# Performance work log

Measured on AMD Instinct MI355X. Metric: run time of the kernel, lower is better.

Reference implementation:

```python
import jax, jax.numpy as jnp
import numpy as np

EMBED_DIM = 384
HEADS = 6
HEAD_DIM = EMBED_DIM // HEADS
WINDOW = 64
B, T, M = 256, 256, 128


def setup_inputs() -> dict:
    key = jax.random.key(0)
    ks = jax.random.split(key, 7)
    s = 0.02
    return {
        "x": jax.random.normal(ks[0], (B, T, EMBED_DIM), dtype=jnp.float32),
        "memory": jax.random.normal(ks[1], (M, EMBED_DIM), dtype=jnp.float32),
        "loss_mask": jnp.ones((B, T), dtype=jnp.float32),
        "qkv_w": jax.random.normal(ks[2], (3 * EMBED_DIM, EMBED_DIM), dtype=jnp.float32) * s,
        "qkv_b": jnp.zeros((3 * EMBED_DIM,), dtype=jnp.float32),
        "proj_w": jax.random.normal(ks[3], (EMBED_DIM, EMBED_DIM), dtype=jnp.float32) * s,
        "proj_b": jnp.zeros((EMBED_DIM,), dtype=jnp.float32),
        "gate": jnp.ones((EMBED_DIM,), dtype=jnp.float32),
    }


def reference(x, memory, loss_mask, qkv_w, qkv_b, proj_w, proj_b, gate):
    Bb, Tt, C = x.shape
    H, D, W = HEADS, HEAD_DIM, WINDOW
    Mm = memory.shape[0]
    T_total = Mm + Tt

    qkv = x @ qkv_w.T + qkv_b                     # [B, T, 3C]
    q, k, v = jnp.split(qkv, 3, axis=-1)
    mem = jnp.broadcast_to(memory[None], (Bb, Mm, C))
    k = jnp.concatenate([mem, k], axis=1)          # [B, M+T, C]
    v = jnp.concatenate([mem, v], axis=1)

    q = q.reshape(Bb, Tt, H, D)
    k = k.reshape(Bb, T_total, H, D)
    v = v.reshape(Bb, T_total, H, D)

    att = jnp.einsum('bthd,bshd->bhts', q, k) * (1.0 / np.sqrt(D))  # [B,H,T,M+T]

    # memory prefix columns are fully attended; self-block is causal AND local-window
    i = jnp.arange(Tt)[:, None]
    j = jnp.arange(Tt)[None, :]
    self_mask = (j <= i) & (jnp.abs(i - j) <= W)   # [T, T]
    full_mask = jnp.concatenate(
        [jnp.ones((Tt, Mm), dtype=bool), self_mask], axis=1)  # [T, M+T]
    att = jnp.where(full_mask[None, None], att, -jnp.inf)
    att = jax.nn.softmax(att, axis=-1)

    out = jnp.einsum('bhts,bshd->bthd', att, v).reshape(Bb, Tt, C)
    out = (out * gate) @ proj_w.T + proj_b
    out = out * loss_mask[..., None]
    return out
```

## Files before the change

kernel.cpp:

```cpp
#include <hip/hip_runtime.h>
#include <hip/hip_bf16.h>

#define Bb 256
#define Tt 256
#define Cc 384
#define Hh 6
#define Dd 64
#define Ww 64
#define Mm 128

typedef short short8 __attribute__((ext_vector_type(8)));
typedef float floatx4 __attribute__((ext_vector_type(4)));

static __device__ __forceinline__ unsigned short f2bf(float f) {
  union { __hip_bfloat16 h; unsigned short u; } cvt;
  cvt.h = __float2bfloat16(f);
  return cvt.u;
}

static __device__ __forceinline__ void gl2lds16(const unsigned short* g, unsigned short* l) {
  __builtin_amdgcn_global_load_lds(
      (const __attribute__((address_space(1))) unsigned int*)(const void*)g,
      (__attribute__((address_space(3))) unsigned int*)(void*)l,
      16, 0, 0);
}


__global__ __launch_bounds__(256) void cvt_x(const float4* __restrict__ x,
                                             ushort4* __restrict__ xb) {
  size_t i = (size_t)blockIdx.x * 256 + threadIdx.x;
  float4 v = x[i];
  ushort4 o;
  o.x = f2bf(v.x); o.y = f2bf(v.y); o.z = f2bf(v.z); o.w = f2bf(v.w);
  xb[i] = o;
}

__global__ __launch_bounds__(256) void cvt_misc(const float* __restrict__ qkv_w,
                                                const float* __restrict__ proj_w,
                                                const float* __restrict__ mem,
                                                unsigned short* __restrict__ wb,
                                                unsigned short* __restrict__ pwb,
                                                unsigned short* __restrict__ memk,
                                                unsigned short* __restrict__ memvt) {
  int i = blockIdx.x * 256 + threadIdx.x;
  wb[i] = f2bf(qkv_w[i]);
  if (i < 147456) pwb[i] = f2bf(proj_w[i]);
  if (i < 49152) {
    int m = i / Cc, c = i % Cc, h = c >> 6, d = c & 63;
    unsigned short bv = f2bf(mem[i]);
    memk[(h * Mm + m) * Dd + d] = bv;
    memvt[(h * Dd + d) * Mm + m] = bv;
  }
}


__global__ __launch_bounds__(256) void gemm_qkv(const unsigned short* __restrict__ xb,
                                                const unsigned short* __restrict__ wb,
                                                const float* __restrict__ qkv_b,
                                                unsigned short* __restrict__ q,
                                                unsigned short* __restrict__ k,
                                                unsigned short* __restrict__ vt)
{
  int tid = threadIdx.x;
  int w = tid >> 6, lane = tid & 63, quad = lane >> 4, l16 = lane & 15;
  int rowbase = blockIdx.y * 128;
  int colbase = blockIdx.x * 128;
  int rowofs = (w >> 1) * 64, colofs = (w & 1) * 64;

  __shared__ __align__(16) unsigned short Alds[128 * 32];
  __shared__ __align__(16) unsigned short Blds[128 * 32];

  int srow = lane >> 2;
  int skc = (lane & 3) * 8;

  floatx4 acc[4][4] = {};
  for (int ks = 0; ks < 12; ++ks) {
    int kk = ks * 32;
#pragma unroll
    for (int c = w; c < 8; c += 4) {
      gl2lds16(xb + (size_t)(rowbase + c * 16 + srow) * 384 + kk + skc,
               &Alds[c * 512 + lane * 8]);
      gl2lds16(wb + (size_t)(colbase + c * 16 + srow) * 384 + kk + skc,
               &Blds[c * 512 + lane * 8]);
    }
    __syncthreads();

    short8 a[4], b[4];
#pragma unroll
    for (int rt = 0; rt < 4; ++rt)
      a[rt] = *reinterpret_cast<const short8*>(&Alds[(rowofs + rt * 16 + l16) * 32 + quad * 8]);
#pragma unroll
    for (int nt = 0; nt < 4; ++nt)
      b[nt] = *reinterpret_cast<const short8*>(&Blds[(colofs + nt * 16 + l16) * 32 + quad * 8]);
#pragma unroll
    for (int rt = 0; rt < 4; ++rt)
#pragma unroll
      for (int nt = 0; nt < 4; ++nt)
        acc[rt][nt] = __builtin_amdgcn_mfma_f32_16x16x32_bf16(a[rt], b[nt], acc[rt][nt], 0, 0, 0);
    __syncthreads();
  }

#pragma unroll
  for (int nt = 0; nt < 4; ++nt) {
    int col = colbase + colofs + nt * 16 + l16;
    int which = col >= 768 ? 2 : (col >= 384 ? 1 : 0);
    int cc = col - which * 384;
    int h = cc >> 6, d = cc & 63;
    float bias = qkv_b[col];
#pragma unroll
    for (int rt = 0; rt < 4; ++rt) {
#pragma unroll
      for (int r = 0; r < 4; ++r) {
        int row = rowbase + rowofs + rt * 16 + quad * 4 + r;
        int bidx = row >> 8, t = row & 255;
        float val = acc[rt][nt][r] + bias;
        size_t bh = (size_t)bidx * Hh + h;
        if (which == 0) {
          q[(bh * Tt + t) * Dd + d] = f2bf(val * 0.125f);
        } else if (which == 1) {
          k[(bh * Tt + t) * Dd + d] = f2bf(val);
        } else {
          vt[(bh * Dd + d) * Tt + t] = f2bf(val);
        }
      }
    }
  }
}

#define PSTRIDE 264

__global__ __launch_bounds__(256, 2) void attn(const unsigned short* __restrict__ q,
                                               const unsigned short* __restrict__ k,
                                               const unsigned short* __restrict__ vt,
                                               const unsigned short* __restrict__ memk,
                                               const unsigned short* __restrict__ memvt,
                                               const float* __restrict__ gate,
                                               unsigned short* __restrict__ aout)
{
  int tq = blockIdx.x, h = blockIdx.y, b = blockIdx.z;
  int t0 = tq * 64;
  int tid = threadIdx.x, w = tid >> 6, lane = tid & 63, quad = lane >> 4, l16 = lane & 15;

  size_t bh = (size_t)b * Hh + h;
  const unsigned short* qp = q + (bh * Tt + t0 + w * 16) * Dd;
  const unsigned short* kp = k + bh * Tt * Dd;
  const unsigned short* vp = vt + bh * Dd * Tt;
  const unsigned short* mkp = memk + (size_t)h * Mm * Dd;
  const unsigned short* mvp = memvt + (size_t)h * Dd * Mm;

  __shared__ __align__(16) unsigned short lds[33280];
  unsigned short* Kmem = lds;
  unsigned short* Kwin = lds + 8192;
  unsigned short* Pb   = lds;
  unsigned short* Vmem = lds + 16896;
  unsigned short* Vwin = lds + 25088;
  unsigned short* pw = Pb + w * 16 * PSTRIDE;

  short8 qa[2];
#pragma unroll
  for (int ks = 0; ks < 2; ++ks)
    qa[ks] = *reinterpret_cast<const short8*>(qp + l16 * Dd + ks * 32 + quad * 8);

#pragma unroll
  for (int i = 0; i < 4; ++i) {
    int G = (i * 4 + w) * 64;
    int g = G + lane;
    int r = g >> 3, cs = g & 7;
    int c = cs ^ (r & 7);
    gl2lds16(mkp + r * 64 + c * 8, Kmem + G * 8 + lane * 8);
  }
#pragma unroll
  for (int i = 0; i < 4; ++i) {
    int G = (i * 4 + w) * 64;
    int g = G + lane;
    int r = g >> 3, cs = g & 7;
    int c = cs ^ (r & 7);
    int j = t0 - 64 + r;
    if (j < 0) j = 0;
    gl2lds16(kp + (size_t)j * 64 + c * 8, Kwin + G * 8 + lane * 8);
  }
#pragma unroll
  for (int i = 0; i < 4; ++i) {
    int G = (i * 4 + w) * 64;
    int g = G + lane;
    int d = g >> 4, cs = g & 15;
    int c = (cs & 8) | ((cs & 7) ^ (d & 7));
    gl2lds16(mvp + d * Mm + c * 8, Vmem + G * 8 + lane * 8);
  }
#pragma unroll
  for (int i = 0; i < 4; ++i) {
    int G = (i * 4 + w) * 64;
    int g = G + lane;
    int d = g >> 4, cs = g & 15;
    int c = (cs & 8) | ((cs & 7) ^ (d & 7));
    int j0 = t0 - 64 + c * 8;
    if (j0 < 0) j0 = 0;
    gl2lds16(vp + (size_t)d * Tt + j0, Vwin + G * 8 + lane * 8);
  }
  __syncthreads();

  floatx4 s[16] = {};

#pragma unroll
  for (int ct = 0; ct < 8; ++ct)
#pragma unroll
    for (int ks = 0; ks < 2; ++ks) {
      int slot = (ks * 4 + quad) ^ (l16 & 7);
      short8 bf = *reinterpret_cast<const short8*>(Kmem + (ct * 16 + l16) * 64 + slot * 8);
      s[ct] = __builtin_amdgcn_mfma_f32_16x16x32_bf16(qa[ks], bf, s[ct], 0, 0, 0);
    }
#pragma unroll
  for (int ct = 0; ct < 8; ++ct) {
    if (ct >= w && ct <= w + 4) {
#pragma unroll
      for (int ks = 0; ks < 2; ++ks) {
        int slot = (ks * 4 + quad) ^ (l16 & 7);
        short8 bf = *reinterpret_cast<const short8*>(Kwin + (ct * 16 + l16) * 64 + slot * 8);
        s[8 + ct] = __builtin_amdgcn_mfma_f32_16x16x32_bf16(qa[ks], bf, s[8 + ct], 0, 0, 0);
      }
    }
  }
  __syncthreads();

#pragma unroll
  for (int ct = 8; ct < 16; ++ct) {
    int j = t0 - 64 + (ct - 8) * 16 + l16;
#pragma unroll
    for (int r = 0; r < 4; ++r) {
      int i = t0 + w * 16 + quad * 4 + r;
      bool valid = (j >= 0) && (j <= i) && (i - j <= 64);
      if (!valid) s[ct][r] = -1e30f;
    }
  }

  float rm[4], rs[4], inv[4];
#pragma unroll
  for (int r = 0; r < 4; ++r) {
    float m = -1e30f;
#pragma unroll
    for (int ct = 0; ct < 16; ++ct) m = fmaxf(m, s[ct][r]);
    rm[r] = m;
  }
#pragma unroll
  for (int off = 1; off < 16; off <<= 1)
#pragma unroll
    for (int r = 0; r < 4; ++r) rm[r] = fmaxf(rm[r], __shfl_xor(rm[r], off, 64));
#pragma unroll
  for (int r = 0; r < 4; ++r) {
    float sum = 0.f;
#pragma unroll
    for (int ct = 0; ct < 16; ++ct) {
      float p = __expf(s[ct][r] - rm[r]);
      s[ct][r] = p;
      sum += p;
    }
    rs[r] = sum;
  }
#pragma unroll
  for (int off = 1; off < 16; off <<= 1)
#pragma unroll
    for (int r = 0; r < 4; ++r) rs[r] += __shfl_xor(rs[r], off, 64);
#pragma unroll
  for (int r = 0; r < 4; ++r) inv[r] = 1.0f / rs[r];

#pragma unroll
  for (int ct = 0; ct < 16; ++ct)
#pragma unroll
    for (int r = 0; r < 4; ++r)
      pw[(quad * 4 + r) * PSTRIDE + ct * 16 + l16] = f2bf(s[ct][r]);

  floatx4 o[4] = {};
#pragma unroll
  for (int ks = 0; ks < 4; ++ks) {
    short8 pa = *reinterpret_cast<const short8*>(pw + l16 * PSTRIDE + ks * 32 + quad * 8);
#pragma unroll
    for (int dt = 0; dt < 4; ++dt) {
      int c0 = ks * 4 + quad;
      int slot = (c0 & 8) | ((c0 & 7) ^ (l16 & 7));
      short8 vb = *reinterpret_cast<const short8*>(Vmem + (dt * 16 + l16) * 128 + slot * 8);
      o[dt] = __builtin_amdgcn_mfma_f32_16x16x32_bf16(pa, vb, o[dt], 0, 0, 0);
    }
  }
#pragma unroll
  for (int ks = 0; ks < 4; ++ks) {
    if (ks >= (w >> 1) && ks <= 2 + (w >> 1)) {
      short8 pa = *reinterpret_cast<const short8*>(pw + l16 * PSTRIDE + (4 + ks) * 32 + quad * 8);
#pragma unroll
      for (int dt = 0; dt < 4; ++dt) {
        int c0 = ks * 4 + quad;
        int slot = (c0 & 8) | ((c0 & 7) ^ (l16 & 7));
        short8 vb = *reinterpret_cast<const short8*>(Vwin + (dt * 16 + l16) * 128 + slot * 8);
        o[dt] = __builtin_amdgcn_mfma_f32_16x16x32_bf16(pa, vb, o[dt], 0, 0, 0);
      }
    }
  }

#pragma unroll
  for (int dt = 0; dt < 4; ++dt) {
    int c = h * 64 + dt * 16 + l16;
    float g = gate[c];
#pragma unroll
    for (int r = 0; r < 4; ++r) {
      int t = t0 + w * 16 + quad * 4 + r;
      float val = o[dt][r] * inv[r] * g;
      aout[((size_t)b * Tt + t) * Cc + c] = f2bf(val);
    }
  }
}


__global__ __launch_bounds__(256) void gemm_proj(const unsigned short* __restrict__ ab,
                                                 const unsigned short* __restrict__ pwb,
                                                 const float* __restrict__ proj_b,
                                                 const float* __restrict__ loss_mask,
                                                 float* __restrict__ out)
{
  int tid = threadIdx.x;
  int w = tid >> 6, lane = tid & 63, quad = lane >> 4, l16 = lane & 15;
  int rowbase = blockIdx.y * 128;
  int colbase = blockIdx.x * 128;
  int rowofs = (w >> 1) * 64, colofs = (w & 1) * 64;

  __shared__ __align__(16) unsigned short Alds[128 * 32];
  __shared__ __align__(16) unsigned short Blds[128 * 32];

  int srow = lane >> 2;
  int skc = (lane & 3) * 8;

  floatx4 acc[4][4] = {};
  for (int ks = 0; ks < 12; ++ks) {
    int kk = ks * 32;
#pragma unroll
    for (int c = w; c < 8; c += 4) {
      gl2lds16(ab + (size_t)(rowbase + c * 16 + srow) * 384 + kk + skc,
               &Alds[c * 512 + lane * 8]);
      gl2lds16(pwb + (size_t)(colbase + c * 16 + srow) * 384 + kk + skc,
               &Blds[c * 512 + lane * 8]);
    }
    __syncthreads();

    short8 a[4], b[4];
#pragma unroll
    for (int rt = 0; rt < 4; ++rt)
      a[rt] = *reinterpret_cast<const short8*>(&Alds[(rowofs + rt * 16 + l16) * 32 + quad * 8]);
#pragma unroll
    for (int nt = 0; nt < 4; ++nt)
      b[nt] = *reinterpret_cast<const short8*>(&Blds[(colofs + nt * 16 + l16) * 32 + quad * 8]);
#pragma unroll
    for (int rt = 0; rt < 4; ++rt)
#pragma unroll
      for (int nt = 0; nt < 4; ++nt)
        acc[rt][nt] = __builtin_amdgcn_mfma_f32_16x16x32_bf16(a[rt], b[nt], acc[rt][nt], 0, 0, 0);
    __syncthreads();
  }

#pragma unroll
  for (int nt = 0; nt < 4; ++nt) {
    int col = colbase + colofs + nt * 16 + l16;
    float bias = proj_b[col];
#pragma unroll
    for (int rt = 0; rt < 4; ++rt) {
#pragma unroll
      for (int r = 0; r < 4; ++r) {
        int row = rowbase + rowofs + rt * 16 + quad * 4 + r;
        float val = (acc[rt][nt][r] + bias) * loss_mask[row];
        out[(size_t)row * 384 + col] = val;
      }
    }
  }
}


extern "C" void kernel_launch(void* const* d_in, const int* in_sizes, int n_in,
                              void* d_out, int out_size, void* d_ws, size_t ws_size,
                              hipStream_t stream) {
  const float* x = (const float*)d_in[0];
  const float* memory = (const float*)d_in[1];
  const float* loss_mask = (const float*)d_in[2];
  const float* qkv_w = (const float*)d_in[3];
  const float* qkv_b = (const float*)d_in[4];
  const float* proj_w = (const float*)d_in[5];
  const float* proj_b = (const float*)d_in[6];
  const float* gate = (const float*)d_in[7];
  float* out = (float*)d_out;

  char* ws = (char*)d_ws;
  unsigned short* xb    = (unsigned short*)(ws + 0);
  unsigned short* qb    = (unsigned short*)(ws + 50331648);
  unsigned short* kb    = (unsigned short*)(ws + 100663296);
  unsigned short* vtb   = (unsigned short*)(ws + 150994944);
  unsigned short* wb    = (unsigned short*)(ws + 201326592);
  unsigned short* pwb   = (unsigned short*)(ws + 202211328);
  unsigned short* memk  = (unsigned short*)(ws + 202506240);
  unsigned short* memvt = (unsigned short*)(ws + 202604544);
  unsigned short* aout  = xb;

  cvt_x<<<dim3(24576), dim3(256), 0, stream>>>((const float4*)x, (ushort4*)xb);
  cvt_misc<<<dim3(1728), dim3(256), 0, stream>>>(qkv_w, proj_w, memory, wb, pwb, memk, memvt);
  gemm_qkv<<<dim3(9, 512), dim3(256), 0, stream>>>(xb, wb, qkv_b, qb, kb, vtb);
  attn<<<dim3(4, 6, 256), dim3(256), 0, stream>>>(qb, kb, vtb, memk, memvt, gate, aout);
  gemm_proj<<<dim3(3, 512), dim3(256), 0, stream>>>(aout, pwb, proj_b, loss_mask, out);
}
```

Before: 468.6 us.

## Double-buffer LDS tiles and remap block IDs in QKV and projection GEMMs

Both GEMM kernels now keep two LDS buffers, so the global-to-LDS load for the next K slice is issued while MFMAs run on the current one. This halves the barriers per K step and hides load latency behind compute. Block indices are also permuted with an XCD-style round-robin remap (orig&7) so blocks that are consecutive in logical order land on the same die and can share L2. LDS use per block doubles, which may reduce occupancy.

Result: faster. 436.7 us (-6.8%).

```diff
diff --git a/kernel.cpp b/kernel.cpp
--- a/kernel.cpp
+++ b/kernel.cpp
@@ -63,40 +63,60 @@
 {
   int tid = threadIdx.x;
   int w = tid >> 6, lane = tid & 63, quad = lane >> 4, l16 = lane & 15;
-  int rowbase = blockIdx.y * 128;
-  int colbase = blockIdx.x * 128;
+
+  int orig = blockIdx.y * 9 + blockIdx.x;
+  int newid = (orig & 7) * 576 + (orig >> 3);
+  int bx = newid % 9, by = newid / 9;
+
+  int rowbase = by * 128;
+  int colbase = bx * 128;
   int rowofs = (w >> 1) * 64, colofs = (w & 1) * 64;
 
-  __shared__ __align__(16) unsigned short Alds[128 * 32];
-  __shared__ __align__(16) unsigned short Blds[128 * 32];
+  __shared__ __align__(16) unsigned short Alds[2][128 * 32];
+  __shared__ __align__(16) unsigned short Blds[2][128 * 32];
 
   int srow = lane >> 2;
   int skc = (lane & 3) * 8;
 
+#define STAGE_QKV(buf, ks_) do {                                                  \
+    int kk = (ks_) * 32;                                                          \
+    _Pragma("unroll")                                                             \
+    for (int c = w; c < 8; c += 4) {                                              \
+      gl2lds16(xb + (size_t)(rowbase + c * 16 + srow) * 384 + kk + skc,           \
+               &Alds[buf][c * 512 + lane * 8]);                                   \
+      gl2lds16(wb + (size_t)(colbase + c * 16 + srow) * 384 + kk + skc,           \
+               &Blds[buf][c * 512 + lane * 8]);                                   \
+    }                                                                             \
+  } while (0)
+
+#define COMPUTE_QKV(buf) do {                                                     \
+    short8 a[4], b[4];                                                            \
+    _Pragma("unroll")                                                             \
+    for (int rt = 0; rt < 4; ++rt)                                                \
+      a[rt] = *reinterpret_cast<const short8*>(                                   \
+          &Alds[buf][(rowofs + rt * 16 + l16) * 32 + quad * 8]);                  \
+    _Pragma("unroll")                                                             \
+    for (int nt = 0; nt < 4; ++nt)                                                \
+      b[nt] = *reinterpret_cast<const short8*>(                                   \
+          &Blds[buf][(colofs + nt * 16 + l16) * 32 + quad * 8]);                  \
+    _Pragma("unroll")                                                             \
+    for (int rt = 0; rt < 4; ++rt)                                                \
+      _Pragma("unroll")                                                           \
+      for (int nt = 0; nt < 4; ++nt)                                              \
+        acc[rt][nt] = __builtin_amdgcn_mfma_f32_16x16x32_bf16(a[rt], b[nt],       \
+                                                              acc[rt][nt], 0, 0, 0); \
+  } while (0)
+
   floatx4 acc[4][4] = {};
-  for (int ks = 0; ks < 12; ++ks) {
-    int kk = ks * 32;
-#pragma unroll
-    for (int c = w; c < 8; c += 4) {
-      gl2lds16(xb + (size_t)(rowbase + c * 16 + srow) * 384 + kk + skc,
-               &Alds[c * 512 + lane * 8]);
-      gl2lds16(wb + (size_t)(colbase + c * 16 + srow) * 384 + kk + skc,
-               &Blds[c * 512 + lane * 8]);
-    }
+  STAGE_QKV(0, 0);
+  __syncthreads();
+#pragma unroll
+  for (int ks = 0; ks < 12; ks += 2) {
+    STAGE_QKV(1, ks + 1);
+    COMPUTE_QKV(0);
     __syncthreads();
-
-    short8 a[4], b[4];
-#pragma unroll
-    for (int rt = 0; rt < 4; ++rt)
-      a[rt] = *reinterpret_cast<const short8*>(&Alds[(rowofs + rt * 16 + l16) * 32 + quad * 8]);
-#pragma unroll
-    for (int nt = 0; nt < 4; ++nt)
-      b[nt] = *reinterpret_cast<const short8*>(&Blds[(colofs + nt * 16 + l16) * 32 + quad * 8]);
-#pragma unroll
-    for (int rt = 0; rt < 4; ++rt)
-#pragma unroll
-      for (int nt = 0; nt < 4; ++nt)
-        acc[rt][nt] = __builtin_amdgcn_mfma_f32_16x16x32_bf16(a[rt], b[nt], acc[rt][nt], 0, 0, 0);
+    if (ks + 2 < 12) STAGE_QKV(0, ks + 2);
+    COMPUTE_QKV(1);
     __syncthreads();
   }
 
@@ -125,6 +145,8 @@
       }
     }
   }
+#undef STAGE_QKV
+#undef COMPUTE_QKV
 }
 
 #define PSTRIDE 264
@@ -317,40 +339,60 @@
 {
   int tid = threadIdx.x;
   int w = tid >> 6, lane = tid & 63, quad = lane >> 4, l16 = lane & 15;
-  int rowbase = blockIdx.y * 128;
-  int colbase = blockIdx.x * 128;
+
+  int orig = blockIdx.y * 3 + blockIdx.x;
+  int newid = (orig & 7) * 192 + (orig >> 3);
+  int bx = newid % 3, by = newid / 3;
+
+  int rowbase = by * 128;
+  int colbase = bx * 128;
   int rowofs = (w >> 1) * 64, colofs = (w & 1) * 64;
 
-  __shared__ __align__(16) unsigned short Alds[128 * 32];
-  __shared__ __align__(16) unsigned short Blds[128 * 32];
+  __shared__ __align__(16) unsigned short Alds[2][128 * 32];
+  __shared__ __align__(16) unsigned short Blds[2][128 * 32];
 
   int srow = lane >> 2;
   int skc = (lane & 3) * 8;
 
+#define STAGE_PROJ(buf, ks_) do {                                                 \
+    int kk = (ks_) * 32;                                                          \
+    _Pragma("unroll")                                                             \
+    for (int c = w; c < 8; c += 4) {                                              \
+      gl2lds16(ab + (size_t)(rowbase + c * 16 + srow) * 384 + kk + skc,           \
+               &Alds[buf][c * 512 + lane * 8]);                                   \
+      gl2lds16(pwb + (size_t)(colbase + c * 16 + srow) * 384 + kk + skc,          \
+               &Blds[buf][c * 512 + lane * 8]);                                   \
+    }                                                                             \
+  } while (0)
+
+#define COMPUTE_PROJ(buf) do {                                                    \
+    short8 a[4], b[4];                                                            \
+    _Pragma("unroll")                                                             \
+    for (int rt = 0; rt < 4; ++rt)                                                \
+      a[rt] = *reinterpret_cast<const short8*>(                                   \
+          &Alds[buf][(rowofs + rt * 16 + l16) * 32 + quad * 8]);                  \
+    _Pragma("unroll")                                                             \
+    for (int nt = 0; nt < 4; ++nt)                                                \
+      b[nt] = *reinterpret_cast<const short8*>(                                   \
+          &Blds[buf][(colofs + nt * 16 + l16) * 32 + quad * 8]);                  \
+    _Pragma("unroll")                                                             \
+    for (int rt = 0; rt < 4; ++rt)                                                \
+      _Pragma("unroll")                                                           \
+      for (int nt = 0; nt < 4; ++nt)                                              \
+        acc[rt][nt] = __builtin_amdgcn_mfma_f32_16x16x32_bf16(a[rt], b[nt],       \
+                                                              acc[rt][nt], 0, 0, 0); \
+  } while (0)
+
   floatx4 acc[4][4] = {};
-  for (int ks = 0; ks < 12; ++ks) {
-    int kk = ks * 32;
-#pragma unroll
-    for (int c = w; c < 8; c += 4) {
-      gl2lds16(ab + (size_t)(rowbase + c * 16 + srow) * 384 + kk + skc,
-               &Alds[c * 512 + lane * 8]);
-      gl2lds16(pwb + (size_t)(colbase + c * 16 + srow) * 384 + kk + skc,
-               &Blds[c * 512 + lane * 8]);
-    }
+  STAGE_PROJ(0, 0);
+  __syncthreads();
+#pragma unroll
+  for (int ks = 0; ks < 12; ks += 2) {
+    STAGE_PROJ(1, ks + 1);
+    COMPUTE_PROJ(0);
     __syncthreads();
-
-    short8 a[4], b[4];
-#pragma unroll
-    for (int rt = 0; rt < 4; ++rt)
-      a[rt] = *reinterpret_cast<const short8*>(&Alds[(rowofs + rt * 16 + l16) * 32 + quad * 8]);
-#pragma unroll
-    for (int nt = 0; nt < 4; ++nt)
-      b[nt] = *reinterpret_cast<const short8*>(&Blds[(colofs + nt * 16 + l16) * 32 + quad * 8]);
-#pragma unroll
-    for (int rt = 0; rt < 4; ++rt)
-#pragma unroll
-      for (int nt = 0; nt < 4; ++nt)
-        acc[rt][nt] = __builtin_amdgcn_mfma_f32_16x16x32_bf16(a[rt], b[nt], acc[rt][nt], 0, 0, 0);
+    if (ks + 2 < 12) STAGE_PROJ(0, ks + 2);
+    COMPUTE_PROJ(1);
     __syncthreads();
   }
 
@@ -368,6 +410,8 @@
       }
     }
   }
+#undef STAGE_PROJ
+#undef COMPUTE_PROJ
 }
 
 
```

## Restructure QKV and proj GEMMs with resident full-K weight tile and swizzled LDS

Applied to the files above, without the earlier changes.

Both GEMMs now load the whole 128-column by full-K weight tile into LDS once per block and stream 64-row activation tiles. The next A tile is prefetched while the epilogue stores run. LDS uses an XOR swizzle to avoid bank conflicts, blocks grow to 512 threads with setprio around the MFMA loops, and block IDs are remapped for XCD-aware scheduling. This cuts per-k-step barriers and repeated weight loads, at the cost of about 144KB of LDS per block, which limits occupancy to one block per CU.

Measured after the change: 446.3 us. -4.8%, faster.

```diff
diff --git a/kernel.cpp b/kernel.cpp
--- a/kernel.cpp
+++ b/kernel.cpp
@@ -24,6 +24,9 @@
       (__attribute__((address_space(3))) unsigned int*)(void*)l,
       16, 0, 0);
 }
+
+#define VW(N) asm volatile("s_waitcnt vmcnt(" #N ")" ::: "memory")
+#define BAR() __builtin_amdgcn_s_barrier()
 
 
 __global__ __launch_bounds__(256) void cvt_x(const float4* __restrict__ x,
@@ -54,7 +57,7 @@
 }
 
 
-__global__ __launch_bounds__(256) void gemm_qkv(const unsigned short* __restrict__ xb,
+__global__ __launch_bounds__(512) void gemm_qkv(const unsigned short* __restrict__ xb,
                                                 const unsigned short* __restrict__ wb,
                                                 const float* __restrict__ qkv_b,
                                                 unsigned short* __restrict__ q,
@@ -63,67 +66,98 @@
 {
   int tid = threadIdx.x;
   int w = tid >> 6, lane = tid & 63, quad = lane >> 4, l16 = lane & 15;
-  int rowbase = blockIdx.y * 128;
-  int colbase = blockIdx.x * 128;
-  int rowofs = (w >> 1) * 64, colofs = (w & 1) * 64;
-
-  __shared__ __align__(16) unsigned short Alds[128 * 32];
-  __shared__ __align__(16) unsigned short Blds[128 * 32];
-
-  int srow = lane >> 2;
-  int skc = (lane & 3) * 8;
-
-  floatx4 acc[4][4] = {};
-  for (int ks = 0; ks < 12; ++ks) {
-    int kk = ks * 32;
-#pragma unroll
-    for (int c = w; c < 8; c += 4) {
-      gl2lds16(xb + (size_t)(rowbase + c * 16 + srow) * 384 + kk + skc,
-               &Alds[c * 512 + lane * 8]);
-      gl2lds16(wb + (size_t)(colbase + c * 16 + srow) * 384 + kk + skc,
-               &Blds[c * 512 + lane * 8]);
-    }
-    __syncthreads();
-
-    short8 a[4], b[4];
-#pragma unroll
-    for (int rt = 0; rt < 4; ++rt)
-      a[rt] = *reinterpret_cast<const short8*>(&Alds[(rowofs + rt * 16 + l16) * 32 + quad * 8]);
-#pragma unroll
-    for (int nt = 0; nt < 4; ++nt)
-      b[nt] = *reinterpret_cast<const short8*>(&Blds[(colofs + nt * 16 + l16) * 32 + quad * 8]);
-#pragma unroll
-    for (int rt = 0; rt < 4; ++rt)
-#pragma unroll
-      for (int nt = 0; nt < 4; ++nt)
-        acc[rt][nt] = __builtin_amdgcn_mfma_f32_16x16x32_bf16(a[rt], b[nt], acc[rt][nt], 0, 0, 0);
-    __syncthreads();
-  }
-
-#pragma unroll
-  for (int nt = 0; nt < 4; ++nt) {
-    int col = colbase + colofs + nt * 16 + l16;
-    int which = col >= 768 ? 2 : (col >= 384 ? 1 : 0);
-    int cc = col - which * 384;
-    int h = cc >> 6, d = cc & 63;
-    float bias = qkv_b[col];
-#pragma unroll
-    for (int rt = 0; rt < 4; ++rt) {
-#pragma unroll
-      for (int r = 0; r < 4; ++r) {
-        int row = rowbase + rowofs + rt * 16 + quad * 4 + r;
-        int bidx = row >> 8, t = row & 255;
-        float val = acc[rt][nt][r] + bias;
-        size_t bh = (size_t)bidx * Hh + h;
-        if (which == 0) {
-          q[(bh * Tt + t) * Dd + d] = f2bf(val * 0.125f);
-        } else if (which == 1) {
-          k[(bh * Tt + t) * Dd + d] = f2bf(val);
-        } else {
-          vt[(bh * Dd + d) * Tt + t] = f2bf(val);
+
+  int id = blockIdx.y * 9 + blockIdx.x;
+  int orig = (id & 7) * 288 + (id >> 3);
+  int bx = orig % 9, by = orig / 9;
+  int colbase = bx * 128;
+  int rowbase0 = by * 256;
+  int rowofs = (w >> 2) * 32, colofs = (w & 3) * 32;
+
+  __shared__ __align__(16) unsigned short Bl[49152];
+  __shared__ __align__(16) unsigned short Al[24576];
+
+#pragma unroll
+  for (int i = 0; i < 12; ++i) {
+    int G = i * 512 + tid;
+    int kg = G >> 10, g = G & 1023;
+    int col = g >> 3, cs = g & 7, c = cs ^ (col & 7);
+    gl2lds16(wb + (size_t)(colbase + col) * 384 + kg * 64 + c * 8, Bl + G * 8);
+  }
+#pragma unroll
+  for (int i = 0; i < 6; ++i) {
+    int G = i * 512 + tid;
+    int kg = G >> 9, g = G & 511;
+    int r = g >> 3, cs = g & 7, c = cs ^ (r & 7);
+    gl2lds16(xb + (size_t)(rowbase0 + r) * 384 + kg * 64 + c * 8, Al + G * 8);
+  }
+  VW(0); BAR();
+
+#pragma unroll
+  for (int t = 0; t < 4; ++t) {
+    floatx4 acc[2][2] = {};
+    __builtin_amdgcn_s_setprio(1);
+#pragma unroll
+    for (int kg = 0; kg < 6; ++kg) {
+#pragma unroll
+      for (int ks = 0; ks < 2; ++ks) {
+        int slot = ((ks * 4 + quad) ^ (l16 & 7)) * 8;
+        short8 a[2], b[2];
+#pragma unroll
+        for (int rt = 0; rt < 2; ++rt)
+          a[rt] = *reinterpret_cast<const short8*>(
+              &Al[kg * 4096 + (rowofs + rt * 16 + l16) * 64 + slot]);
+#pragma unroll
+        for (int nt = 0; nt < 2; ++nt)
+          b[nt] = *reinterpret_cast<const short8*>(
+              &Bl[kg * 8192 + (colofs + nt * 16 + l16) * 64 + slot]);
+#pragma unroll
+        for (int rt = 0; rt < 2; ++rt)
+#pragma unroll
+          for (int nt = 0; nt < 2; ++nt)
+            acc[rt][nt] = __builtin_amdgcn_mfma_f32_16x16x32_bf16(a[rt], b[nt],
+                                                                  acc[rt][nt], 0, 0, 0);
+      }
+    }
+    __builtin_amdgcn_s_setprio(0);
+    BAR();
+    if (t < 3) {
+      int rb = rowbase0 + (t + 1) * 64;
+#pragma unroll
+      for (int i = 0; i < 6; ++i) {
+        int G = i * 512 + tid;
+        int kg = G >> 9, g = G & 511;
+        int r = g >> 3, cs = g & 7, c = cs ^ (r & 7);
+        gl2lds16(xb + (size_t)(rb + r) * 384 + kg * 64 + c * 8, Al + G * 8);
+      }
+    }
+    int rowb = rowbase0 + t * 64 + rowofs;
+#pragma unroll
+    for (int nt = 0; nt < 2; ++nt) {
+      int col = colbase + colofs + nt * 16 + l16;
+      int which = col >= 768 ? 2 : (col >= 384 ? 1 : 0);
+      int cc = col - which * 384;
+      int h = cc >> 6, d = cc & 63;
+      float bias = qkv_b[col];
+#pragma unroll
+      for (int rt = 0; rt < 2; ++rt) {
+#pragma unroll
+        for (int r = 0; r < 4; ++r) {
+          int row = rowb + rt * 16 + quad * 4 + r;
+          int bidx = row >> 8, tt = row & 255;
+          float val = acc[rt][nt][r] + bias;
+          size_t bh = (size_t)bidx * Hh + h;
+          if (which == 0) {
+            q[(bh * Tt + tt) * Dd + d] = f2bf(val * 0.125f);
+          } else if (which == 1) {
+            k[(bh * Tt + tt) * Dd + d] = f2bf(val);
+          } else {
+            vt[(bh * Dd + d) * Tt + tt] = f2bf(val);
+          }
         }
       }
     }
+    if (t < 3) { VW(16); BAR(); }
   }
 }
 
@@ -309,7 +343,7 @@
 }
 
 
-__global__ __launch_bounds__(256) void gemm_proj(const unsigned short* __restrict__ ab,
+__global__ __launch_bounds__(512) void gemm_proj(const unsigned short* __restrict__ ab,
                                                  const unsigned short* __restrict__ pwb,
                                                  const float* __restrict__ proj_b,
                                                  const float* __restrict__ loss_mask,
@@ -317,56 +351,87 @@
 {
   int tid = threadIdx.x;
   int w = tid >> 6, lane = tid & 63, quad = lane >> 4, l16 = lane & 15;
-  int rowbase = blockIdx.y * 128;
-  int colbase = blockIdx.x * 128;
-  int rowofs = (w >> 1) * 64, colofs = (w & 1) * 64;
-
-  __shared__ __align__(16) unsigned short Alds[128 * 32];
-  __shared__ __align__(16) unsigned short Blds[128 * 32];
-
-  int srow = lane >> 2;
-  int skc = (lane & 3) * 8;
-
-  floatx4 acc[4][4] = {};
-  for (int ks = 0; ks < 12; ++ks) {
-    int kk = ks * 32;
-#pragma unroll
-    for (int c = w; c < 8; c += 4) {
-      gl2lds16(ab + (size_t)(rowbase + c * 16 + srow) * 384 + kk + skc,
-               &Alds[c * 512 + lane * 8]);
-      gl2lds16(pwb + (size_t)(colbase + c * 16 + srow) * 384 + kk + skc,
-               &Blds[c * 512 + lane * 8]);
-    }
-    __syncthreads();
-
-    short8 a[4], b[4];
-#pragma unroll
-    for (int rt = 0; rt < 4; ++rt)
-      a[rt] = *reinterpret_cast<const short8*>(&Alds[(rowofs + rt * 16 + l16) * 32 + quad * 8]);
-#pragma unroll
-    for (int nt = 0; nt < 4; ++nt)
-      b[nt] = *reinterpret_cast<const short8*>(&Blds[(colofs + nt * 16 + l16) * 32 + quad * 8]);
-#pragma unroll
-    for (int rt = 0; rt < 4; ++rt)
-#pragma unroll
-      for (int nt = 0; nt < 4; ++nt)
-        acc[rt][nt] = __builtin_amdgcn_mfma_f32_16x16x32_bf16(a[rt], b[nt], acc[rt][nt], 0, 0, 0);
-    __syncthreads();
-  }
-
-#pragma unroll
-  for (int nt = 0; nt < 4; ++nt) {
-    int col = colbase + colofs + nt * 16 + l16;
-    float bias = proj_b[col];
-#pragma unroll
-    for (int rt = 0; rt < 4; ++rt) {
-#pragma unroll
-      for (int r = 0; r < 4; ++r) {
-        int row = rowbase + rowofs + rt * 16 + quad * 4 + r;
-        float val = (acc[rt][nt][r] + bias) * loss_mask[row];
-        out[(size_t)row * 384 + col] = val;
-      }
-    }
+
+  int id = blockIdx.y * 3 + blockIdx.x;
+  int orig = (id & 7) * 192 + (id >> 3);
+  int bx = orig % 3, by = orig / 3;
+  int colbase = bx * 128;
+  int rowbase0 = by * 128;
+  int rowofs = (w >> 2) * 32, colofs = (w & 3) * 32;
+
+  __shared__ __align__(16) unsigned short Bl[49152];
+  __shared__ __align__(16) unsigned short Al[24576];
+
+#pragma unroll
+  for (int i = 0; i < 12; ++i) {
+    int G = i * 512 + tid;
+    int kg = G >> 10, g = G & 1023;
+    int col = g >> 3, cs = g & 7, c = cs ^ (col & 7);
+    gl2lds16(pwb + (size_t)(colbase + col) * 384 + kg * 64 + c * 8, Bl + G * 8);
+  }
+#pragma unroll
+  for (int i = 0; i < 6; ++i) {
+    int G = i * 512 + tid;
+    int kg = G >> 9, g = G & 511;
+    int r = g >> 3, cs = g & 7, c = cs ^ (r & 7);
+    gl2lds16(ab + (size_t)(rowbase0 + r) * 384 + kg * 64 + c * 8, Al + G * 8);
+  }
+  VW(0); BAR();
+
+#pragma unroll
+  for (int t = 0; t < 2; ++t) {
+    floatx4 acc[2][2] = {};
+    __builtin_amdgcn_s_setprio(1);
+#pragma unroll
+    for (int kg = 0; kg < 6; ++kg) {
+#pragma unroll
+      for (int ks = 0; ks < 2; ++ks) {
+        int slot = ((ks * 4 + quad) ^ (l16 & 7)) * 8;
+        short8 a[2], b[2];
+#pragma unroll
+        for (int rt = 0; rt < 2; ++rt)
+          a[rt] = *reinterpret_cast<const short8*>(
+              &Al[kg * 4096 + (rowofs + rt * 16 + l16) * 64 + slot]);
+#pragma unroll
+        for (int nt = 0; nt < 2; ++nt)
+          b[nt] = *reinterpret_cast<const short8*>(
+              &Bl[kg * 8192 + (colofs + nt * 16 + l16) * 64 + slot]);
+#pragma unroll
+        for (int rt = 0; rt < 2; ++rt)
+#pragma unroll
+          for (int nt = 0; nt < 2; ++nt)
+            acc[rt][nt] = __builtin_amdgcn_mfma_f32_16x16x32_bf16(a[rt], b[nt],
+                                                                  acc[rt][nt], 0, 0, 0);
+      }
+    }
+    __builtin_amdgcn_s_setprio(0);
+    BAR();
+    if (t < 1) {
+      int rb = rowbase0 + 64;
+#pragma unroll
+      for (int i = 0; i < 6; ++i) {
+        int G = i * 512 + tid;
+        int kg = G >> 9, g = G & 511;
+        int r = g >> 3, cs = g & 7, c = cs ^ (r & 7);
+        gl2lds16(ab + (size_t)(rb + r) * 384 + kg * 64 + c * 8, Al + G * 8);
+      }
+    }
+    int rowb = rowbase0 + t * 64 + rowofs;
+#pragma unroll
+    for (int nt = 0; nt < 2; ++nt) {
+      int col = colbase + colofs + nt * 16 + l16;
+      float bias = proj_b[col];
+#pragma unroll
+      for (int rt = 0; rt < 2; ++rt) {
+#pragma unroll
+        for (int r = 0; r < 4; ++r) {
+          int row = rowb + rt * 16 + quad * 4 + r;
+          float val = (acc[rt][nt][r] + bias) * loss_mask[row];
+          out[(size_t)row * 384 + col] = val;
+        }
+      }
+    }
+    if (t < 1) { VW(16); BAR(); }
   }
 }
 
@@ -397,7 +462,7 @@
 
   cvt_x<<<dim3(24576), dim3(256), 0, stream>>>((const float4*)x, (ushort4*)xb);
   cvt_misc<<<dim3(1728), dim3(256), 0, stream>>>(qkv_w, proj_w, memory, wb, pwb, memk, memvt);
-  gemm_qkv<<<dim3(9, 512), dim3(256), 0, stream>>>(xb, wb, qkv_b, qb, kb, vtb);
+  gemm_qkv<<<dim3(9, 256), dim3(512), 0, stream>>>(xb, wb, qkv_b, qb, kb, vtb);
   attn<<<dim3(4, 6, 256), dim3(256), 0, stream>>>(qb, kb, vtb, memk, memvt, gate, aout);
-  gemm_proj<<<dim3(3, 512), dim3(256), 0, stream>>>(aout, pwb, proj_b, loss_mask, out);
-}
+  gemm_proj<<<dim3(3, 512), dim3(512), 0, stream>>>(aout, pwb, proj_b, loss_mask, out);
+}
```

## Restructure QKV and projection GEMMs with resident weight tiles and register-streamed A

Applied to the files above, without the earlier changes.

Both GEMMs now use 512-thread blocks that keep a full 64-column by 384-K weight slab in LDS. The slab is loaded once with an XOR swizzle to avoid bank conflicts. Each wave streams its own 64-row A tile straight from global memory into registers, prefetched two K-steps ahead, which removes the per-K-step LDS staging and barriers. Block IDs are remapped so neighbouring blocks share weight columns, and MFMA sections get raised priority. In exchange, each block uses more LDS and registers, and the uncoalesced direct global A loads could hurt bandwidth.

Result: slower. 493.1 us (+5.2%).

```diff
diff --git a/kernel.cpp b/kernel.cpp
--- a/kernel.cpp
+++ b/kernel.cpp
@@ -24,6 +24,9 @@
       (__attribute__((address_space(3))) unsigned int*)(void*)l,
       16, 0, 0);
 }
+
+#define VW(N) asm volatile("s_waitcnt vmcnt(" #N ")" ::: "memory")
+#define BAR() __builtin_amdgcn_s_barrier()
 
 
 __global__ __launch_bounds__(256) void cvt_x(const float4* __restrict__ x,
@@ -54,7 +57,7 @@
 }
 
 
-__global__ __launch_bounds__(256) void gemm_qkv(const unsigned short* __restrict__ xb,
+__global__ __launch_bounds__(512) void gemm_qkv(const unsigned short* __restrict__ xb,
                                                 const unsigned short* __restrict__ wb,
                                                 const float* __restrict__ qkv_b,
                                                 unsigned short* __restrict__ q,
@@ -63,46 +66,69 @@
 {
   int tid = threadIdx.x;
   int w = tid >> 6, lane = tid & 63, quad = lane >> 4, l16 = lane & 15;
-  int rowbase = blockIdx.y * 128;
-  int colbase = blockIdx.x * 128;
-  int rowofs = (w >> 1) * 64, colofs = (w & 1) * 64;
-
-  __shared__ __align__(16) unsigned short Alds[128 * 32];
-  __shared__ __align__(16) unsigned short Blds[128 * 32];
-
-  int srow = lane >> 2;
-  int skc = (lane & 3) * 8;
+
+  int id = blockIdx.y * 18 + blockIdx.x;
+  int orig = (id & 7) * 288 + (id >> 3);
+  int bx = orig % 18, by = orig / 18;
+  int colbase = bx * 64;
+  int rowbase = by * 512 + w * 64;
+
+  __shared__ __align__(16) unsigned short Bl[24576];
+
+  short8 a[3][4];
+#pragma unroll
+  for (int rt = 0; rt < 4; ++rt)
+    a[0][rt] = *reinterpret_cast<const short8*>(
+        xb + (size_t)(rowbase + rt * 16 + l16) * 384 + 0 * 32 + quad * 8);
+#pragma unroll
+  for (int rt = 0; rt < 4; ++rt)
+    a[1][rt] = *reinterpret_cast<const short8*>(
+        xb + (size_t)(rowbase + rt * 16 + l16) * 384 + 1 * 32 + quad * 8);
+
+#pragma unroll
+  for (int i = 0; i < 6; ++i) {
+    int G = i * 512 + tid;
+    int col = G / 48, cs = G % 48;
+    int c = (cs & 0x38) | ((cs & 7) ^ (col & 7));
+    gl2lds16(wb + (size_t)(colbase + col) * 384 + c * 8, Bl + G * 8);
+  }
+  VW(0); BAR();
 
   floatx4 acc[4][4] = {};
-  for (int ks = 0; ks < 12; ++ks) {
-    int kk = ks * 32;
-#pragma unroll
-    for (int c = w; c < 8; c += 4) {
-      gl2lds16(xb + (size_t)(rowbase + c * 16 + srow) * 384 + kk + skc,
-               &Alds[c * 512 + lane * 8]);
-      gl2lds16(wb + (size_t)(colbase + c * 16 + srow) * 384 + kk + skc,
-               &Blds[c * 512 + lane * 8]);
-    }
-    __syncthreads();
-
-    short8 a[4], b[4];
-#pragma unroll
-    for (int rt = 0; rt < 4; ++rt)
-      a[rt] = *reinterpret_cast<const short8*>(&Alds[(rowofs + rt * 16 + l16) * 32 + quad * 8]);
-#pragma unroll
-    for (int nt = 0; nt < 4; ++nt)
-      b[nt] = *reinterpret_cast<const short8*>(&Blds[(colofs + nt * 16 + l16) * 32 + quad * 8]);
-#pragma unroll
-    for (int rt = 0; rt < 4; ++rt)
-#pragma unroll
-      for (int nt = 0; nt < 4; ++nt)
-        acc[rt][nt] = __builtin_amdgcn_mfma_f32_16x16x32_bf16(a[rt], b[nt], acc[rt][nt], 0, 0, 0);
-    __syncthreads();
-  }
+
+#define STEP_QKV(kk) do {                                                         \
+    if ((kk) + 2 < 12) {                                                          \
+      _Pragma("unroll")                                                           \
+      for (int rt = 0; rt < 4; ++rt)                                              \
+        a[((kk) + 2) % 3][rt] = *reinterpret_cast<const short8*>(                 \
+            xb + (size_t)(rowbase + rt * 16 + l16) * 384 + ((kk) + 2) * 32 + quad * 8); \
+    }                                                                             \
+    short8 b[4];                                                                  \
+    _Pragma("unroll")                                                             \
+    for (int nt = 0; nt < 4; ++nt) {                                              \
+      int kc = (kk) * 4 + quad;                                                   \
+      int col = nt * 16 + l16;                                                    \
+      int slot = (kc & 0x38) | ((kc & 7) ^ (col & 7));                            \
+      b[nt] = *reinterpret_cast<const short8*>(&Bl[col * 384 + slot * 8]);        \
+    }                                                                             \
+    __builtin_amdgcn_s_setprio(1);                                                \
+    _Pragma("unroll")                                                             \
+    for (int rt = 0; rt < 4; ++rt)                                                \
+      _Pragma("unroll")                                                           \
+      for (int nt = 0; nt < 4; ++nt)                                              \
+        acc[rt][nt] = __builtin_amdgcn_mfma_f32_16x16x32_bf16(a[(kk) % 3][rt],    \
+                          b[nt], acc[rt][nt], 0, 0, 0);                           \
+    __builtin_amdgcn_s_setprio(0);                                                \
+  } while (0)
+
+  STEP_QKV(0);  STEP_QKV(1);  STEP_QKV(2);  STEP_QKV(3);
+  STEP_QKV(4);  STEP_QKV(5);  STEP_QKV(6);  STEP_QKV(7);
+  STEP_QKV(8);  STEP_QKV(9);  STEP_QKV(10); STEP_QKV(11);
+#undef STEP_QKV
 
 #pragma unroll
   for (int nt = 0; nt < 4; ++nt) {
-    int col = colbase + colofs + nt * 16 + l16;
+    int col = colbase + nt * 16 + l16;
     int which = col >= 768 ? 2 : (col >= 384 ? 1 : 0);
     int cc = col - which * 384;
     int h = cc >> 6, d = cc & 63;
@@ -111,16 +137,16 @@
     for (int rt = 0; rt < 4; ++rt) {
 #pragma unroll
       for (int r = 0; r < 4; ++r) {
-        int row = rowbase + rowofs + rt * 16 + quad * 4 + r;
-        int bidx = row >> 8, t = row & 255;
+        int row = rowbase + rt * 16 + quad * 4 + r;
+        int bidx = row >> 8, tt = row & 255;
         float val = acc[rt][nt][r] + bias;
         size_t bh = (size_t)bidx * Hh + h;
         if (which == 0) {
-          q[(bh * Tt + t) * Dd + d] = f2bf(val * 0.125f);
+          q[(bh * Tt + tt) * Dd + d] = f2bf(val * 0.125f);
         } else if (which == 1) {
-          k[(bh * Tt + t) * Dd + d] = f2bf(val);
+          k[(bh * Tt + tt) * Dd + d] = f2bf(val);
         } else {
-          vt[(bh * Dd + d) * Tt + t] = f2bf(val);
+          vt[(bh * Dd + d) * Tt + tt] = f2bf(val);
         }
       }
     }
@@ -309,7 +335,7 @@
 }
 
 
-__global__ __launch_bounds__(256) void gemm_proj(const unsigned short* __restrict__ ab,
+__global__ __launch_bounds__(512) void gemm_proj(const unsigned short* __restrict__ ab,
                                                  const unsigned short* __restrict__ pwb,
                                                  const float* __restrict__ proj_b,
                                                  const float* __restrict__ loss_mask,
@@ -317,52 +343,75 @@
 {
   int tid = threadIdx.x;
   int w = tid >> 6, lane = tid & 63, quad = lane >> 4, l16 = lane & 15;
-  int rowbase = blockIdx.y * 128;
-  int colbase = blockIdx.x * 128;
-  int rowofs = (w >> 1) * 64, colofs = (w & 1) * 64;
-
-  __shared__ __align__(16) unsigned short Alds[128 * 32];
-  __shared__ __align__(16) unsigned short Blds[128 * 32];
-
-  int srow = lane >> 2;
-  int skc = (lane & 3) * 8;
+
+  int id = blockIdx.y * 6 + blockIdx.x;
+  int orig = (id & 7) * 96 + (id >> 3);
+  int bx = orig % 6, by = orig / 6;
+  int colbase = bx * 64;
+  int rowbase = by * 512 + w * 64;
+
+  __shared__ __align__(16) unsigned short Bl[24576];
+
+  short8 a[3][4];
+#pragma unroll
+  for (int rt = 0; rt < 4; ++rt)
+    a[0][rt] = *reinterpret_cast<const short8*>(
+        ab + (size_t)(rowbase + rt * 16 + l16) * 384 + 0 * 32 + quad * 8);
+#pragma unroll
+  for (int rt = 0; rt < 4; ++rt)
+    a[1][rt] = *reinterpret_cast<const short8*>(
+        ab + (size_t)(rowbase + rt * 16 + l16) * 384 + 1 * 32 + quad * 8);
+
+#pragma unroll
+  for (int i = 0; i < 6; ++i) {
+    int G = i * 512 + tid;
+    int col = G / 48, cs = G % 48;
+    int c = (cs & 0x38) | ((cs & 7) ^ (col & 7));
+    gl2lds16(pwb + (size_t)(colbase + col) * 384 + c * 8, Bl + G * 8);
+  }
+  VW(0); BAR();
 
   floatx4 acc[4][4] = {};
-  for (int ks = 0; ks < 12; ++ks) {
-    int kk = ks * 32;
-#pragma unroll
-    for (int c = w; c < 8; c += 4) {
-      gl2lds16(ab + (size_t)(rowbase + c * 16 + srow) * 384 + kk + skc,
-               &Alds[c * 512 + lane * 8]);
-      gl2lds16(pwb + (size_t)(colbase + c * 16 + srow) * 384 + kk + skc,
-               &Blds[c * 512 + lane * 8]);
-    }
-    __syncthreads();
-
-    short8 a[4], b[4];
-#pragma unroll
-    for (int rt = 0; rt < 4; ++rt)
-      a[rt] = *reinterpret_cast<const short8*>(&Alds[(rowofs + rt * 16 + l16) * 32 + quad * 8]);
-#pragma unroll
-    for (int nt = 0; nt < 4; ++nt)
-      b[nt] = *reinterpret_cast<const short8*>(&Blds[(colofs + nt * 16 + l16) * 32 + quad * 8]);
-#pragma unroll
-    for (int rt = 0; rt < 4; ++rt)
-#pragma unroll
-      for (int nt = 0; nt < 4; ++nt)
-        acc[rt][nt] = __builtin_amdgcn_mfma_f32_16x16x32_bf16(a[rt], b[nt], acc[rt][nt], 0, 0, 0);
-    __syncthreads();
-  }
+
+#define STEP_PROJ(kk) do {                                                        \
+    if ((kk) + 2 < 12) {                                                          \
+      _Pragma("unroll")                                                           \
+      for (int rt = 0; rt < 4; ++rt)                                              \
+        a[((kk) + 2) % 3][rt] = *reinterpret_cast<const short8*>(                 \
+            ab + (size_t)(rowbase + rt * 16 + l16) * 384 + ((kk) + 2) * 32 + quad * 8); \
+    }                                                                             \
+    short8 b[4];                                                                  \
+    _Pragma("unroll")                                                             \
+    for (int nt = 0; nt < 4; ++nt) {                                              \
+      int kc = (kk) * 4 + quad;                                                   \
+      int col = nt * 16 + l16;                                                    \
+      int slot = (kc & 0x38) | ((kc & 7) ^ (col & 7));                            \
+      b[nt] = *reinterpret_cast<const short8*>(&Bl[col * 384 + slot * 8]);        \
+    }                                                                             \
+    __builtin_amdgcn_s_setprio(1);                                                \
+    _Pragma("unroll")                                                             \
+    for (int rt = 0; rt < 4; ++rt)                                                \
+      _Pragma("unroll")                                                           \
+      for (int nt = 0; nt < 4; ++nt)                                              \
+        acc[rt][nt] = __builtin_amdgcn_mfma_f32_16x16x32_bf16(a[(kk) % 3][rt],    \
+                          b[nt], acc[rt][nt], 0, 0, 0);                           \
+    __builtin_amdgcn_s_setprio(0);                                                \
+  } while (0)
+
+  STEP_PROJ(0);  STEP_PROJ(1);  STEP_PROJ(2);  STEP_PROJ(3);
+  STEP_PROJ(4);  STEP_PROJ(5);  STEP_PROJ(6);  STEP_PROJ(7);
+  STEP_PROJ(8);  STEP_PROJ(9);  STEP_PROJ(10); STEP_PROJ(11);
+#undef STEP_PROJ
 
 #pragma unroll
   for (int nt = 0; nt < 4; ++nt) {
-    int col = colbase + colofs + nt * 16 + l16;
+    int col = colbase + nt * 16 + l16;
     float bias = proj_b[col];
 #pragma unroll
     for (int rt = 0; rt < 4; ++rt) {
 #pragma unroll
       for (int r = 0; r < 4; ++r) {
-        int row = rowbase + rowofs + rt * 16 + quad * 4 + r;
+        int row = rowbase + rt * 16 + quad * 4 + r;
         float val = (acc[rt][nt][r] + bias) * loss_mask[row];
         out[(size_t)row * 384 + col] = val;
       }
@@ -397,7 +446,7 @@
 
   cvt_x<<<dim3(24576), dim3(256), 0, stream>>>((const float4*)x, (ushort4*)xb);
   cvt_misc<<<dim3(1728), dim3(256), 0, stream>>>(qkv_w, proj_w, memory, wb, pwb, memk, memvt);
-  gemm_qkv<<<dim3(9, 512), dim3(256), 0, stream>>>(xb, wb, qkv_b, qb, kb, vtb);
+  gemm_qkv<<<dim3(18, 128), dim3(512), 0, stream>>>(xb, wb, qkv_b, qb, kb, vtb);
   attn<<<dim3(4, 6, 256), dim3(256), 0, stream>>>(qb, kb, vtb, memk, memvt, gate, aout);
-  gemm_proj<<<dim3(3, 512), dim3(256), 0, stream>>>(aout, pwb, proj_b, loss_mask, out);
-}
+  gemm_proj<<<dim3(6, 128), dim3(512), 0, stream>>>(aout, pwb, proj_b, loss_mask, out);
+}
```
